# Kernel tuning notes

Hardware: AMD Instinct MI355X
Metric: run time of the kernel (lower is better)

The kernel has to match this reference:

```python
import jax, jax.numpy as jnp
import numpy as np

EPS = 1e-6
NUM_HEADS = 16
ROPE_THETA = 100000.0


def _rope_tables(seq_len, head_dim, theta):
    inv_freq = 1.0 / (theta ** (np.arange(0, head_dim, 2, dtype=np.float32) / head_dim))
    t = np.arange(seq_len, dtype=np.float32)
    freqs = np.outer(t, inv_freq)                      # (S, head_dim//2)
    emb = np.concatenate([freqs, freqs], axis=-1)      # (S, head_dim)
    return jnp.asarray(np.cos(emb))[None], jnp.asarray(np.sin(emb))[None]  # (1,S,D)


def setup_inputs() -> dict:
    key = jax.random.key(0)
    ks = jax.random.split(key, 6)
    B, S, H = 2, 2048, 1024
    head_dim = H // NUM_HEADS
    cos, sin = _rope_tables(S, head_dim, ROPE_THETA)
    scale = 0.02
    return {
        "hidden_states": jax.random.normal(ks[0], (B, S, H), dtype=jnp.float32),
        "cos": cos, "sin": sin,
        "Wq": jax.random.normal(ks[1], (H, H), dtype=jnp.float32) * scale,
        "bq": jnp.zeros((H,), dtype=jnp.float32),
        "Wk": jax.random.normal(ks[2], (H, H), dtype=jnp.float32) * scale,
        "bk": jnp.zeros((H,), dtype=jnp.float32),
        "Wv": jax.random.normal(ks[3], (H, H), dtype=jnp.float32) * scale,
        "bv": jnp.zeros((H,), dtype=jnp.float32),
        "Wo": jax.random.normal(ks[4], (H, H), dtype=jnp.float32) * scale,
        "bo": jnp.zeros((H,), dtype=jnp.float32),
        "rms_weight": jnp.ones((H,), dtype=jnp.float32),
    }


def _rms_norm(x, w):
    var = jnp.mean(x * x, axis=-1, keepdims=True)
    return x * jax.lax.rsqrt(var + EPS) * w


def _rotate_half(x):
    x1, x2 = jnp.split(x, 2, axis=-1)
    return jnp.concatenate([-x2, x1], axis=-1)


def reference(hidden_states, cos, sin, Wq, bq, Wk, bk, Wv, bv, Wo, bo, rms_weight):
    B, S, H = hidden_states.shape
    D = H // NUM_HEADS
    q = hidden_states @ Wq.T + bq
    k = hidden_states @ Wk.T + bk
    v = hidden_states @ Wv.T + bv
    # RMSNorm over full hidden dim BEFORE head split (as in original)
    q = _rms_norm(q, rms_weight)
    k = _rms_norm(k, rms_weight)
    # (B,S,H) -> (B,heads,S,D)
    q = q.reshape(B, S, NUM_HEADS, D).transpose(0, 2, 1, 3)
    k = k.reshape(B, S, NUM_HEADS, D).transpose(0, 2, 1, 3)
    v = v.reshape(B, S, NUM_HEADS, D).transpose(0, 2, 1, 3)
    # RoPE: cos/sin (1,S,D) -> unsqueeze head dim
    c = cos[:, None, :, :]
    s = sin[:, None, :, :]
    q = q * c + _rotate_half(q) * s
    k = k * c + _rotate_half(k) * s
    # attention (faithful: boolean tril mask is ADDED as 0/1, not -inf)
    scale = D ** 0.5
    scores = jnp.einsum("bhqd,bhkd->bhqk", q, k) / scale
    mask = jnp.tril(jnp.ones((S, S), dtype=scores.dtype))  # +1 on causal, +0 elsewhere
    attn = jax.nn.softmax(scores + mask, axis=-1)
    out = jnp.einsum("bhqk,bhkd->bhqd", attn, v)
    out = out.transpose(0, 2, 1, 3).reshape(B, S, H)
    return out @ Wo.T + bo
```

## Files before the change

kernel.cpp:

```cpp
#include <hip/hip_runtime.h>

typedef unsigned short u16;
typedef __attribute__((ext_vector_type(8))) _Float16 half8;
typedef __attribute__((ext_vector_type(2))) __fp16 fp16x2;
typedef __attribute__((ext_vector_type(4))) float f32x4;

#define MFMAH(A,B,C) __builtin_amdgcn_mfma_f32_16x16x32_f16(A,B,C,0,0,0)
#define LOG2E 1.4426950408889634f
#define C1 0.18033688011112042f

__device__ __forceinline__ u16 f2h(float f){
  _Float16 h = (_Float16)f; u16 r; __builtin_memcpy(&r,&h,2); return r;
}
__device__ __forceinline__ float h2f(u16 v){
  _Float16 h; __builtin_memcpy(&h,&v,2); return (float)h;
}
__device__ __forceinline__ unsigned int pack_h2(float a, float b){
  fp16x2 h = __builtin_amdgcn_cvt_pkrtz(a,b);
  unsigned int r; __builtin_memcpy(&r,&h,4); return r;
}

__device__ __forceinline__ void async_ld16(const void* g, void* l) {
  __builtin_amdgcn_global_load_lds(
      (const __attribute__((address_space(1))) unsigned int*)g,
      (__attribute__((address_space(3))) unsigned int*)l, 16, 0, 0);
}

__global__ __launch_bounds__(256) void cast_all(const float* __restrict__ hs,
    const float* __restrict__ wq, const float* __restrict__ wk,
    const float* __restrict__ wv, const float* __restrict__ wo,
    u16* __restrict__ dst)
{
  unsigned int i = blockIdx.x*256 + threadIdx.x;
  size_t el = (size_t)i * 8;
  const float* src; size_t off;
  if (el < 4194304) { src = hs; off = el; }
  else {
    unsigned int r = (unsigned int)((el - 4194304) >> 20);
    src = (r==0)?wq:(r==1)?wk:(r==2)?wv:wo;
    off = (el - 4194304) & 1048575;
  }
  float4 a = *reinterpret_cast<const float4*>(src+off);
  float4 b = *reinterpret_cast<const float4*>(src+off+4);
  uint4 o = {pack_h2(a.x,a.y), pack_h2(a.z,a.w), pack_h2(b.x,b.y), pack_h2(b.z,b.w)};
  *reinterpret_cast<uint4*>(dst + el) = o;
}

__global__ __launch_bounds__(256) void gemm_qkv(const u16* __restrict__ A,
                                                const u16* __restrict__ W,
                                                const float* __restrict__ b0p,
                                                const float* __restrict__ b1p,
                                                const float* __restrict__ b2p,
                                                u16* __restrict__ out,
                                                int M, int N, int K)
{
  __shared__ __align__(16) u16 lds_a[128*32];
  __shared__ __align__(16) u16 lds_w[128*32];
  const int t = threadIdx.x;
  const int lane = t & 63, wave = t >> 6;
  const int wm = wave >> 1, wn = wave & 1;
  const int lr = lane & 15, quad = lane >> 4;
  const int n0 = blockIdx.x * 128, m0 = blockIdx.y * 128;
  const int wbase = t & 192;

  const f32x4 fzero = {0.f,0.f,0.f,0.f};
  f32x4 acc[4][4];
  #pragma unroll
  for (int i=0;i<4;++i)
    #pragma unroll
    for (int j=0;j<4;++j) acc[i][j] = fzero;

  for (int k0 = 0; k0 < K; k0 += 32) {
    __syncthreads();
    #pragma unroll
    for (int it=0; it<2; ++it) {
      int idx = it*256 + t;
      int row = idx >> 2, c8 = (idx & 3) * 8;
      int lbase = (it*256 + wbase) * 8;
      async_ld16(&A[(size_t)(m0+row)*K + k0 + c8], &lds_a[lbase]);
      async_ld16(&W[(size_t)(n0+row)*K + k0 + c8], &lds_w[lbase]);
    }
    __syncthreads();
    half8 af[4], bfr[4];
    #pragma unroll
    for (int mt=0; mt<4; ++mt)
      af[mt] = *reinterpret_cast<const half8*>(&lds_a[(wm*64 + mt*16 + lr)*32 + quad*8]);
    #pragma unroll
    for (int nt=0; nt<4; ++nt)
      bfr[nt] = *reinterpret_cast<const half8*>(&lds_w[(wn*64 + nt*16 + lr)*32 + quad*8]);
    #pragma unroll
    for (int mt=0; mt<4; ++mt)
      #pragma unroll
      for (int nt=0; nt<4; ++nt)
        acc[mt][nt] = MFMAH(af[mt], bfr[nt], acc[mt][nt]);
  }

  int which = n0 >> 10;
  const float* bp = (which==0) ? b0p : (which==1) ? b1p : b2p;
  u16* dst = out + (size_t)which * 4194304;
  if (which == 2) {
    #pragma unroll
    for (int nt=0; nt<4; ++nt) {
      int nn = (n0 & 1023) + wn*64 + nt*16 + lr;
      float bv = bp[nn];
      int hh = nn >> 6, d = nn & 63;
      #pragma unroll
      for (int mt=0; mt<4; ++mt) {
        int m = m0 + wm*64 + mt*16 + quad*4;
        int b = m >> 11, s = m & 2047;
        uint2 o = {pack_h2(acc[mt][nt][0]+bv, acc[mt][nt][1]+bv),
                   pack_h2(acc[mt][nt][2]+bv, acc[mt][nt][3]+bv)};
        *reinterpret_cast<uint2*>(&dst[((size_t)(b*16 + hh)*64 + d)*2048 + s]) = o;
      }
    }
  } else {
    #pragma unroll
    for (int nt=0; nt<4; ++nt) {
      int nn = (n0 & 1023) + wn*64 + nt*16 + lr;
      float bv = bp[nn];
      int hh = nn >> 6, d = nn & 63;
      #pragma unroll
      for (int mt=0; mt<4; ++mt)
        #pragma unroll
        for (int r=0; r<4; ++r) {
          int m = m0 + wm*64 + mt*16 + quad*4 + r;
          int b = m >> 11, s = m & 2047;
          dst[((size_t)(b*16 + hh) * 2048 + s) * 64 + d] = f2h(acc[mt][nt][r] + bv);
        }
    }
  }
}

__global__ __launch_bounds__(256) void gemm_o(const u16* __restrict__ A,
                                              const u16* __restrict__ W,
                                              const float* __restrict__ bias,
                                              float* __restrict__ O,
                                              int M, int N, int K)
{
  __shared__ __align__(16) u16 lds_a[128*32];
  __shared__ __align__(16) u16 lds_w[64*32];
  const int t = threadIdx.x;
  const int lane = t & 63, wm = t >> 6;
  const int lr = lane & 15, quad = lane >> 4;
  const int n0 = blockIdx.x * 64, m0 = blockIdx.y * 128;
  const int wbase = t & 192;

  const f32x4 fzero = {0.f,0.f,0.f,0.f};
  f32x4 acc[2][4];
  #pragma unroll
  for (int i=0;i<2;++i)
    #pragma unroll
    for (int j=0;j<4;++j) acc[i][j] = fzero;

  for (int k0 = 0; k0 < K; k0 += 32) {
    __syncthreads();
    #pragma unroll
    for (int it=0; it<2; ++it) {
      int idx = it*256 + t;
      int row = idx >> 2, c8 = (idx & 3) * 8;
      int lbase = (it*256 + wbase) * 8;
      async_ld16(&A[(size_t)(m0+row)*K + k0 + c8], &lds_a[lbase]);
    }
    async_ld16(&W[(size_t)(n0 + (t>>2))*K + k0 + (t&3)*8], &lds_w[wbase*8]);
    __syncthreads();
    half8 af[2], bfr[4];
    #pragma unroll
    for (int mt=0; mt<2; ++mt)
      af[mt] = *reinterpret_cast<const half8*>(&lds_a[(wm*32 + mt*16 + lr)*32 + quad*8]);
    #pragma unroll
    for (int nt=0; nt<4; ++nt)
      bfr[nt] = *reinterpret_cast<const half8*>(&lds_w[(nt*16 + lr)*32 + quad*8]);
    #pragma unroll
    for (int mt=0; mt<2; ++mt)
      #pragma unroll
      for (int nt=0; nt<4; ++nt)
        acc[mt][nt] = MFMAH(af[mt], bfr[nt], acc[mt][nt]);
  }

  #pragma unroll
  for (int nt=0; nt<4; ++nt) {
    int n = n0 + nt*16 + lr;
    float bv = bias[n];
    #pragma unroll
    for (int mt=0; mt<2; ++mt)
      #pragma unroll
      for (int r=0; r<4; ++r) {
        int m = m0 + wm*32 + mt*16 + quad*4 + r;
        O[(size_t)m * N + n] = acc[mt][nt][r] + bv;
      }
  }
}

__global__ __launch_bounds__(256) void rmsrope(u16* __restrict__ qb, u16* __restrict__ kb,
                                               const float* __restrict__ cosb,
                                               const float* __restrict__ sinb,
                                               const float* __restrict__ w)
{
  u16* buf = blockIdx.y ? kb : qb;
  const int bs = blockIdx.x;
  const int b = bs >> 11, s = bs & 2047;
  const int t = threadIdx.x;
  float x1[2], x2[2];
  float ss = 0.f;
  #pragma unroll
  for (int i=0;i<2;++i){
    int p = t + i*256;
    int h = p >> 5, d = p & 31;
    size_t base = ((size_t)(b*16+h)*2048 + s)*64;
    x1[i] = h2f(buf[base + d]);
    x2[i] = h2f(buf[base + d + 32]);
    ss += x1[i]*x1[i] + x2[i]*x2[i];
  }
  #pragma unroll
  for (int off=32; off>0; off>>=1) ss += __shfl_xor(ss, off, 64);
  __shared__ float red[4];
  if ((t & 63) == 0) red[t>>6] = ss;
  __syncthreads();
  float tot = red[0]+red[1]+red[2]+red[3];
  float r = rsqrtf(tot * (1.0f/1024.0f) + 1e-6f);
  #pragma unroll
  for (int i=0;i<2;++i){
    int p = t + i*256;
    int h = p >> 5, d = p & 31;
    size_t base = ((size_t)(b*16+h)*2048 + s)*64;
    float w1 = w[h*64+d], w2 = w[h*64+d+32];
    float n1 = x1[i]*r*w1, n2 = x2[i]*r*w2;
    float c1 = cosb[s*64+d],    s1 = sinb[s*64+d];
    float c2 = cosb[s*64+d+32], s2 = sinb[s*64+d+32];
    buf[base+d]    = f2h(n1*c1 - n2*s1);
    buf[base+d+32] = f2h(n2*c2 + n1*s2);
  }
}

__global__ __launch_bounds__(512) void attn(const u16* __restrict__ qh,
                                            const u16* __restrict__ kh,
                                            const u16* __restrict__ vt,
                                            u16* __restrict__ ao)
{
  __shared__ __align__(16) u16 kbuf[64*72];
  __shared__ __align__(16) u16 vbuf[64*72];
  const int t = threadIdx.x;
  const int lane = t & 63, w = t >> 6;
  const int lr = lane & 15, quad = lane >> 4;
  const int bx = blockIdx.x;
  const int qbase = bx * 128;
  const int bh = blockIdx.y;
  const int b = bh >> 4, h = bh & 15;
  const size_t hb = (size_t)bh * 2048 * 64;
  const u16* qp = qh + hb;
  const u16* kp = kh + hb;
  const u16* vtp = vt + hb;

  const int q_abs = qbase + w*16 + lr;
  half8 qf0 = *reinterpret_cast<const half8*>(&qp[(size_t)q_abs*64 + quad*8]);
  half8 qf1 = *reinterpret_cast<const half8*>(&qp[(size_t)q_abs*64 + 32 + quad*8]);

  const int row = t >> 3;
  const int cc = t & 7;
  const int vu = cc >> 2, vq = cc & 3;
  const int k1 = vu*32 + vq*4;
  u16* kw = &kbuf[row*72 + cc*8];
  u16* vw = &vbuf[row*72 + cc*8];
  const u16* kg = kp + (size_t)row*64 + cc*8;
  const u16* vg = vtp + (size_t)row*2048 + k1;

  const f32x4 fzero = {0.f,0.f,0.f,0.f};
  f32x4 oacc[4];
  #pragma unroll
  for (int i=0;i<4;++i) oacc[i] = fzero;
  float lsum = 0.f;
  const int diag = (qbase + w*16) >> 6;

  for (int kt=0; kt<32; ++kt) {
    __syncthreads();
    {
      uint4 kv = *reinterpret_cast<const uint4*>(kg + (size_t)kt*4096);
      uint2 g1 = *reinterpret_cast<const uint2*>(vg + kt*64);
      uint2 g2 = *reinterpret_cast<const uint2*>(vg + kt*64 + 16);
      *reinterpret_cast<uint4*>(kw) = kv;
      uint4 vv = {g1.x, g1.y, g2.x, g2.y};
      *reinterpret_cast<uint4*>(vw) = vv;
    }
    __syncthreads();

    f32x4 zz[4];
    #pragma unroll
    for (int ksub=0; ksub<4; ++ksub) {
      const u16* kr = &kbuf[(ksub*16+lr)*72 + quad*8];
      half8 a0, a1;
      __builtin_memcpy(&a0, kr, 16);
      __builtin_memcpy(&a1, kr+32, 16);
      f32x4 z = fzero;
      z = MFMAH(a0, qf0, z);
      z = MFMAH(a1, qf1, z);
      zz[ksub] = z;
    }

    unsigned int pk[4][2];
    if (kt != diag) {
      float ml = (kt < diag) ? LOG2E : 0.0f;
      #pragma unroll
      for (int ksub=0; ksub<4; ++ksub) {
        float p0 = __builtin_amdgcn_exp2f(__builtin_fmaf(zz[ksub][0], C1, ml));
        float p1 = __builtin_amdgcn_exp2f(__builtin_fmaf(zz[ksub][1], C1, ml));
        float p2 = __builtin_amdgcn_exp2f(__builtin_fmaf(zz[ksub][2], C1, ml));
        float p3 = __builtin_amdgcn_exp2f(__builtin_fmaf(zz[ksub][3], C1, ml));
        lsum += (p0+p1) + (p2+p3);
        pk[ksub][0] = pack_h2(p0, p1);
        pk[ksub][1] = pack_h2(p2, p3);
      }
    } else {
      #pragma unroll
      for (int ksub=0; ksub<4; ++ksub) {
        int key0 = kt*64 + ksub*16 + quad*4;
        float p[4];
        #pragma unroll
        for (int r=0; r<4; ++r) {
          float ml = (key0 + r <= q_abs) ? LOG2E : 0.0f;
          p[r] = __builtin_amdgcn_exp2f(__builtin_fmaf(zz[ksub][r], C1, ml));
          lsum += p[r];
        }
        pk[ksub][0] = pack_h2(p[0], p[1]);
        pk[ksub][1] = pack_h2(p[2], p[3]);
      }
    }

    #pragma unroll
    for (int u=0; u<2; ++u) {
      uint4 pq = {pk[2*u][0], pk[2*u][1], pk[2*u+1][0], pk[2*u+1][1]};
      half8 pf;
      __builtin_memcpy(&pf, &pq, 16);
      #pragma unroll
      for (int dt=0; dt<4; ++dt) {
        half8 vf;
        __builtin_memcpy(&vf, &vbuf[(dt*16+lr)*72 + u*32 + quad*8], 16);
        oacc[dt] = MFMAH(vf, pf, oacc[dt]);
      }
    }
  }

  lsum += __shfl_xor(lsum, 16, 64);
  lsum += __shfl_xor(lsum, 32, 64);
  float inv = 1.0f / lsum;
  size_t rowbase = ((size_t)(b*2048 + q_abs))*1024 + h*64;
  #pragma unroll
  for (int dt=0; dt<4; ++dt) {
    uint2 o = {pack_h2(oacc[dt][0]*inv, oacc[dt][1]*inv),
               pack_h2(oacc[dt][2]*inv, oacc[dt][3]*inv)};
    *reinterpret_cast<uint2*>(&ao[rowbase + dt*16 + quad*4]) = o;
  }
}

extern "C" void kernel_launch(void* const* d_in, const int* in_sizes, int n_in,
                              void* d_out, int out_size, void* d_ws, size_t ws_size,
                              hipStream_t stream)
{
  const float* hs   = (const float*)d_in[0];
  const float* cosb = (const float*)d_in[1];
  const float* sinb = (const float*)d_in[2];
  const float* Wq   = (const float*)d_in[3];
  const float* bq   = (const float*)d_in[4];
  const float* Wk   = (const float*)d_in[5];
  const float* bk   = (const float*)d_in[6];
  const float* Wv   = (const float*)d_in[7];
  const float* bv   = (const float*)d_in[8];
  const float* Wo   = (const float*)d_in[9];
  const float* bo   = (const float*)d_in[10];
  const float* rw   = (const float*)d_in[11];

  const size_t NEL = (size_t)4096 * 1024;
  const size_t WEL = (size_t)1024 * 1024;
  u16* hsb = (u16*)d_ws;
  u16* wqb = hsb + NEL;
  u16* wob = wqb + 3*WEL;
  u16* qhb = wob + WEL;
  u16* khb = qhb + NEL;
  u16* vtb = khb + NEL;
  u16* aob = hsb;

  cast_all<<<4096, 256, 0, stream>>>(hs, Wq, Wk, Wv, Wo, hsb);
  gemm_qkv<<<dim3(24,32), 256, 0, stream>>>(hsb, wqb, bq, bk, bv, qhb, 4096, 3072, 1024);
  rmsrope<<<dim3(4096,2), 256, 0, stream>>>(qhb, khb, cosb, sinb, rw);
  attn<<<dim3(16,32), 512, 0, stream>>>(qhb, khb, vtb, aob);
  gemm_o<<<dim3(16,32), 256, 0, stream>>>(aob, wob, bo, (float*)d_out, 4096, 1024, 1024);
}
```

Baseline: 237.2 us.

## Vectorize GEMM epilogues, split Q/K from V GEMM, vectorize rmsrope, double-buffer attention

The Q/K GEMM and the output GEMM swap their MFMA operands so each lane holds four contiguous columns, which lets the epilogue write packed uint2/float4 stores instead of scalar ones. The V projection moves into its own kernel that keeps the transposed layout. rmsrope drops to 128 threads, each handling four elements with vector loads and stores. The attention kernel double-buffers its K/V LDS tiles, prefetching the next tile into registers so one barrier per iteration is removed. Together these target uncoalesced stores and load latency, at the cost of an extra kernel launch and twice the LDS in attention.

```diff
diff --git a/kernel.cpp b/kernel.cpp
--- a/kernel.cpp
+++ b/kernel.cpp
@@ -46,13 +46,13 @@
   *reinterpret_cast<uint4*>(dst + el) = o;
 }
 
-__global__ __launch_bounds__(256) void gemm_qkv(const u16* __restrict__ A,
-                                                const u16* __restrict__ W,
-                                                const float* __restrict__ b0p,
-                                                const float* __restrict__ b1p,
-                                                const float* __restrict__ b2p,
-                                                u16* __restrict__ out,
-                                                int M, int N, int K)
+__global__ __launch_bounds__(256) void gemm_qk(const u16* __restrict__ A,
+                                               const u16* __restrict__ W,
+                                               const float* __restrict__ bqp,
+                                               const float* __restrict__ bkp,
+                                               u16* __restrict__ qout,
+                                               u16* __restrict__ kout,
+                                               int M, int N, int K)
 {
   __shared__ __align__(16) u16 lds_a[128*32];
   __shared__ __align__(16) u16 lds_w[128*32];
@@ -92,41 +92,87 @@
     for (int mt=0; mt<4; ++mt)
       #pragma unroll
       for (int nt=0; nt<4; ++nt)
+        acc[mt][nt] = MFMAH(bfr[nt], af[mt], acc[mt][nt]);
+  }
+
+  int which = n0 >> 10;
+  const float* bp = which ? bkp : bqp;
+  u16* dst = which ? kout : qout;
+  #pragma unroll
+  for (int nt=0; nt<4; ++nt) {
+    int nn = (n0 & 1023) + wn*64 + nt*16 + quad*4;
+    float4 bv = *reinterpret_cast<const float4*>(&bp[nn]);
+    int hh = nn >> 6, d4 = nn & 63;
+    #pragma unroll
+    for (int mt=0; mt<4; ++mt) {
+      int m = m0 + wm*64 + mt*16 + lr;
+      int b = m >> 11, s = m & 2047;
+      uint2 o = {pack_h2(acc[mt][nt][0]+bv.x, acc[mt][nt][1]+bv.y),
+                 pack_h2(acc[mt][nt][2]+bv.z, acc[mt][nt][3]+bv.w)};
+      *reinterpret_cast<uint2*>(&dst[((size_t)(b*16 + hh)*2048 + s)*64 + d4]) = o;
+    }
+  }
+}
+
+__global__ __launch_bounds__(256) void gemm_v(const u16* __restrict__ A,
+                                              const u16* __restrict__ W,
+                                              const float* __restrict__ bvp,
+                                              u16* __restrict__ vout,
+                                              int M, int N, int K)
+{
+  __shared__ __align__(16) u16 lds_a[128*32];
+  __shared__ __align__(16) u16 lds_w[128*32];
+  const int t = threadIdx.x;
+  const int lane = t & 63, wave = t >> 6;
+  const int wm = wave >> 1, wn = wave & 1;
+  const int lr = lane & 15, quad = lane >> 4;
+  const int n0 = blockIdx.x * 128, m0 = blockIdx.y * 128;
+  const int wbase = t & 192;
+
+  const f32x4 fzero = {0.f,0.f,0.f,0.f};
+  f32x4 acc[4][4];
+  #pragma unroll
+  for (int i=0;i<4;++i)
+    #pragma unroll
+    for (int j=0;j<4;++j) acc[i][j] = fzero;
+
+  for (int k0 = 0; k0 < K; k0 += 32) {
+    __syncthreads();
+    #pragma unroll
+    for (int it=0; it<2; ++it) {
+      int idx = it*256 + t;
+      int row = idx >> 2, c8 = (idx & 3) * 8;
+      int lbase = (it*256 + wbase) * 8;
+      async_ld16(&A[(size_t)(m0+row)*K + k0 + c8], &lds_a[lbase]);
+      async_ld16(&W[(size_t)(n0+row)*K + k0 + c8], &lds_w[lbase]);
+    }
+    __syncthreads();
+    half8 af[4], bfr[4];
+    #pragma unroll
+    for (int mt=0; mt<4; ++mt)
+      af[mt] = *reinterpret_cast<const half8*>(&lds_a[(wm*64 + mt*16 + lr)*32 + quad*8]);
+    #pragma unroll
+    for (int nt=0; nt<4; ++nt)
+      bfr[nt] = *reinterpret_cast<const half8*>(&lds_w[(wn*64 + nt*16 + lr)*32 + quad*8]);
+    #pragma unroll
+    for (int mt=0; mt<4; ++mt)
+      #pragma unroll
+      for (int nt=0; nt<4; ++nt)
         acc[mt][nt] = MFMAH(af[mt], bfr[nt], acc[mt][nt]);
   }
 
-  int which = n0 >> 10;
-  const float* bp = (which==0) ? b0p : (which==1) ? b1p : b2p;
-  u16* dst = out + (size_t)which * 4194304;
-  if (which == 2) {
-    #pragma unroll
-    for (int nt=0; nt<4; ++nt) {
-      int nn = (n0 & 1023) + wn*64 + nt*16 + lr;
-      float bv = bp[nn];
-      int hh = nn >> 6, d = nn & 63;
-      #pragma unroll
-      for (int mt=0; mt<4; ++mt) {
-        int m = m0 + wm*64 + mt*16 + quad*4;
-        int b = m >> 11, s = m & 2047;
-        uint2 o = {pack_h2(acc[mt][nt][0]+bv, acc[mt][nt][1]+bv),
-                   pack_h2(acc[mt][nt][2]+bv, acc[mt][nt][3]+bv)};
-        *reinterpret_cast<uint2*>(&dst[((size_t)(b*16 + hh)*64 + d)*2048 + s]) = o;
-      }
-    }
-  } else {
-    #pragma unroll
-    for (int nt=0; nt<4; ++nt) {
-      int nn = (n0 & 1023) + wn*64 + nt*16 + lr;
-      float bv = bp[nn];
-      int hh = nn >> 6, d = nn & 63;
-      #pragma unroll
-      for (int mt=0; mt<4; ++mt)
-        #pragma unroll
-        for (int r=0; r<4; ++r) {
-          int m = m0 + wm*64 + mt*16 + quad*4 + r;
-          int b = m >> 11, s = m & 2047;
-          dst[((size_t)(b*16 + hh) * 2048 + s) * 64 + d] = f2h(acc[mt][nt][r] + bv);
-        }
+  #pragma unroll
+  for (int nt=0; nt<4; ++nt) {
+    int nn = n0 + wn*64 + nt*16 + lr;
+    float bv = bvp[nn];
+    int hh = nn >> 6, d = nn & 63;
+    #pragma unroll
+    for (int mt=0; mt<4; ++mt) {
+      int m = m0 + wm*64 + mt*16 + quad*4;
+      int b = m >> 11, s = m & 2047;
+      uint2 o = {pack_h2(acc[mt][nt][0]+bv, acc[mt][nt][1]+bv),
+                 pack_h2(acc[mt][nt][2]+bv, acc[mt][nt][3]+bv)};
+      *reinterpret_cast<uint2*>(&vout[((size_t)(b*16 + hh)*64 + d)*2048 + s]) = o;
     }
   }
 }
@@ -174,24 +220,24 @@
     for (int mt=0; mt<2; ++mt)
       #pragma unroll
       for (int nt=0; nt<4; ++nt)
-        acc[mt][nt] = MFMAH(af[mt], bfr[nt], acc[mt][nt]);
+        acc[mt][nt] = MFMAH(bfr[nt], af[mt], acc[mt][nt]);
   }
 
   #pragma unroll
   for (int nt=0; nt<4; ++nt) {
-    int n = n0 + nt*16 + lr;
-    float bv = bias[n];
-    #pragma unroll
-    for (int mt=0; mt<2; ++mt)
-      #pragma unroll
-      for (int r=0; r<4; ++r) {
-        int m = m0 + wm*32 + mt*16 + quad*4 + r;
-        O[(size_t)m * N + n] = acc[mt][nt][r] + bv;
-      }
-  }
-}
-
-__global__ __launch_bounds__(256) void rmsrope(u16* __restrict__ qb, u16* __restrict__ kb,
+    int nb = n0 + nt*16 + quad*4;
+    float4 bv = *reinterpret_cast<const float4*>(&bias[nb]);
+    #pragma unroll
+    for (int mt=0; mt<2; ++mt) {
+      int m = m0 + wm*32 + mt*16 + lr;
+      float4 o = {acc[mt][nt][0]+bv.x, acc[mt][nt][1]+bv.y,
+                  acc[mt][nt][2]+bv.z, acc[mt][nt][3]+bv.w};
+      *reinterpret_cast<float4*>(&O[(size_t)m * N + nb]) = o;
+    }
+  }
+}
+
+__global__ __launch_bounds__(128) void rmsrope(u16* __restrict__ qb, u16* __restrict__ kb,
                                                const float* __restrict__ cosb,
                                                const float* __restrict__ sinb,
                                                const float* __restrict__ w)
@@ -200,36 +246,44 @@
   const int bs = blockIdx.x;
   const int b = bs >> 11, s = bs & 2047;
   const int t = threadIdx.x;
-  float x1[2], x2[2];
+  const int h = t >> 3, d0 = (t & 7) * 4;
+  size_t base = ((size_t)(b*16+h)*2048 + s)*64;
+
+  uint2 u1 = *reinterpret_cast<const uint2*>(&buf[base + d0]);
+  uint2 u2 = *reinterpret_cast<const uint2*>(&buf[base + d0 + 32]);
+  u16 a1[4], a2[4];
+  __builtin_memcpy(a1, &u1, 8); __builtin_memcpy(a2, &u2, 8);
+  float x1[4], x2[4];
   float ss = 0.f;
   #pragma unroll
-  for (int i=0;i<2;++i){
-    int p = t + i*256;
-    int h = p >> 5, d = p & 31;
-    size_t base = ((size_t)(b*16+h)*2048 + s)*64;
-    x1[i] = h2f(buf[base + d]);
-    x2[i] = h2f(buf[base + d + 32]);
-    ss += x1[i]*x1[i] + x2[i]*x2[i];
+  for (int j=0;j<4;++j){
+    x1[j] = h2f(a1[j]); x2[j] = h2f(a2[j]);
+    ss += x1[j]*x1[j] + x2[j]*x2[j];
   }
   #pragma unroll
   for (int off=32; off>0; off>>=1) ss += __shfl_xor(ss, off, 64);
-  __shared__ float red[4];
+  __shared__ float red[2];
   if ((t & 63) == 0) red[t>>6] = ss;
   __syncthreads();
-  float tot = red[0]+red[1]+red[2]+red[3];
+  float tot = red[0] + red[1];
   float r = rsqrtf(tot * (1.0f/1024.0f) + 1e-6f);
-  #pragma unroll
-  for (int i=0;i<2;++i){
-    int p = t + i*256;
-    int h = p >> 5, d = p & 31;
-    size_t base = ((size_t)(b*16+h)*2048 + s)*64;
-    float w1 = w[h*64+d], w2 = w[h*64+d+32];
-    float n1 = x1[i]*r*w1, n2 = x2[i]*r*w2;
-    float c1 = cosb[s*64+d],    s1 = sinb[s*64+d];
-    float c2 = cosb[s*64+d+32], s2 = sinb[s*64+d+32];
-    buf[base+d]    = f2h(n1*c1 - n2*s1);
-    buf[base+d+32] = f2h(n2*c2 + n1*s2);
-  }
+
+  float4 w1 = *reinterpret_cast<const float4*>(&w[h*64+d0]);
+  float4 w2 = *reinterpret_cast<const float4*>(&w[h*64+d0+32]);
+  float4 c1 = *reinterpret_cast<const float4*>(&cosb[s*64+d0]);
+  float4 s1 = *reinterpret_cast<const float4*>(&sinb[s*64+d0]);
+  float4 c2 = *reinterpret_cast<const float4*>(&cosb[s*64+d0+32]);
+  float4 s2 = *reinterpret_cast<const float4*>(&sinb[s*64+d0+32]);
+  float n1[4] = {x1[0]*r*w1.x, x1[1]*r*w1.y, x1[2]*r*w1.z, x1[3]*r*w1.w};
+  float n2[4] = {x2[0]*r*w2.x, x2[1]*r*w2.y, x2[2]*r*w2.z, x2[3]*r*w2.w};
+  float o1[4] = {n1[0]*c1.x - n2[0]*s1.x, n1[1]*c1.y - n2[1]*s1.y,
+                 n1[2]*c1.z - n2[2]*s1.z, n1[3]*c1.w - n2[3]*s1.w};
+  float o2[4] = {n2[0]*c2.x + n1[0]*s2.x, n2[1]*c2.y + n1[1]*s2.y,
+                 n2[2]*c2.z + n1[2]*s2.z, n2[3]*c2.w + n1[3]*s2.w};
+  uint2 v1 = {pack_h2(o1[0],o1[1]), pack_h2(o1[2],o1[3])};
+  uint2 v2 = {pack_h2(o2[0],o2[1]), pack_h2(o2[2],o2[3])};
+  *reinterpret_cast<uint2*>(&buf[base + d0])      = v1;
+  *reinterpret_cast<uint2*>(&buf[base + d0 + 32]) = v2;
 }
 
 __global__ __launch_bounds__(512) void attn(const u16* __restrict__ qh,
@@ -237,8 +291,8 @@
                                             const u16* __restrict__ vt,
                                             u16* __restrict__ ao)
 {
-  __shared__ __align__(16) u16 kbuf[64*72];
-  __shared__ __align__(16) u16 vbuf[64*72];
+  __shared__ __align__(16) u16 kbuf[2][64*72];
+  __shared__ __align__(16) u16 vbuf[2][64*72];
   const int t = threadIdx.x;
   const int lane = t & 63, w = t >> 6;
   const int lr = lane & 15, quad = lane >> 4;
@@ -259,8 +313,7 @@
   const int cc = t & 7;
   const int vu = cc >> 2, vq = cc & 3;
   const int k1 = vu*32 + vq*4;
-  u16* kw = &kbuf[row*72 + cc*8];
-  u16* vw = &vbuf[row*72 + cc*8];
+  const int kofs = row*72 + cc*8;
   const u16* kg = kp + (size_t)row*64 + cc*8;
   const u16* vg = vtp + (size_t)row*2048 + k1;
 
@@ -271,22 +324,30 @@
   float lsum = 0.f;
   const int diag = (qbase + w*16) >> 6;
 
+  {
+    uint4 kv = *reinterpret_cast<const uint4*>(kg);
+    uint2 g1 = *reinterpret_cast<const uint2*>(vg);
+    uint2 g2 = *reinterpret_cast<const uint2*>(vg + 16);
+    *reinterpret_cast<uint4*>(&kbuf[0][kofs]) = kv;
+    uint4 vv = {g1.x, g1.y, g2.x, g2.y};
+    *reinterpret_cast<uint4*>(&vbuf[0][kofs]) = vv;
+  }
+
   for (int kt=0; kt<32; ++kt) {
-    __syncthreads();
-    {
-      uint4 kv = *reinterpret_cast<const uint4*>(kg + (size_t)kt*4096);
-      uint2 g1 = *reinterpret_cast<const uint2*>(vg + kt*64);
-      uint2 g2 = *reinterpret_cast<const uint2*>(vg + kt*64 + 16);
-      *reinterpret_cast<uint4*>(kw) = kv;
-      uint4 vv = {g1.x, g1.y, g2.x, g2.y};
-      *reinterpret_cast<uint4*>(vw) = vv;
-    }
-    __syncthreads();
+    uint4 kvn; uint2 g1n, g2n;
+    if (kt < 31) {
+      kvn = *reinterpret_cast<const uint4*>(kg + (size_t)(kt+1)*4096);
+      g1n = *reinterpret_cast<const uint2*>(vg + (kt+1)*64);
+      g2n = *reinterpret_cast<const uint2*>(vg + (kt+1)*64 + 16);
+    }
+    __syncthreads();
+    const u16* kb = kbuf[kt & 1];
+    const u16* vb = vbuf[kt & 1];
 
     f32x4 zz[4];
     #pragma unroll
     for (int ksub=0; ksub<4; ++ksub) {
-      const u16* kr = &kbuf[(ksub*16+lr)*72 + quad*8];
+      const u16* kr = &kb[(ksub*16+lr)*72 + quad*8];
       half8 a0, a1;
       __builtin_memcpy(&a0, kr, 16);
       __builtin_memcpy(&a1, kr+32, 16);
@@ -333,9 +394,15 @@
       #pragma unroll
       for (int dt=0; dt<4; ++dt) {
         half8 vf;
-        __builtin_memcpy(&vf, &vbuf[(dt*16+lr)*72 + u*32 + quad*8], 16);
+        __builtin_memcpy(&vf, &vb[(dt*16+lr)*72 + u*32 + quad*8], 16);
         oacc[dt] = MFMAH(vf, pf, oacc[dt]);
       }
+    }
+
+    if (kt < 31) {
+      *reinterpret_cast<uint4*>(&kbuf[(kt+1)&1][kofs]) = kvn;
+      uint4 vv = {g1n.x, g1n.y, g2n.x, g2n.y};
+      *reinterpret_cast<uint4*>(&vbuf[(kt+1)&1][kofs]) = vv;
     }
   }
 
@@ -372,6 +439,7 @@
   const size_t WEL = (size_t)1024 * 1024;
   u16* hsb = (u16*)d_ws;
   u16* wqb = hsb + NEL;
+  u16* wvb = wqb + 2*WEL;
   u16* wob = wqb + 3*WEL;
   u16* qhb = wob + WEL;
   u16* khb = qhb + NEL;
@@ -379,8 +447,9 @@
   u16* aob = hsb;
 
   cast_all<<<4096, 256, 0, stream>>>(hs, Wq, Wk, Wv, Wo, hsb);
-  gemm_qkv<<<dim3(24,32), 256, 0, stream>>>(hsb, wqb, bq, bk, bv, qhb, 4096, 3072, 1024);
-  rmsrope<<<dim3(4096,2), 256, 0, stream>>>(qhb, khb, cosb, sinb, rw);
+  gemm_qk<<<dim3(16,32), 256, 0, stream>>>(hsb, wqb, bq, bk, qhb, khb, 4096, 2048, 1024);
+  gemm_v<<<dim3(8,32), 256, 0, stream>>>(hsb, wvb, bv, vtb, 4096, 1024, 1024);
+  rmsrope<<<dim3(4096,2), 128, 0, stream>>>(qhb, khb, cosb, sinb, rw);
   attn<<<dim3(16,32), 512, 0, stream>>>(qhb, khb, vtb, aob);
   gemm_o<<<dim3(16,32), 256, 0, stream>>>(aob, wob, bo, (float*)d_out, 4096, 1024, 1024);
 }
```

New measurement: 234.5 us. About the same (-1.1%).
